# Kernel tuning notes

Hardware: AMD Instinct MI355X
Metric: run time of the kernel (lower is better)

Reference implementation:

```python
import jax, jax.numpy as jnp
import numpy as np

P, Q = 4, 16            # mlp_quad_last_shape
N, D_IN, H = 100000, 3, 256
N_QUAD = 128


def setup_inputs() -> dict:
    key = jax.random.key(0)
    ks = jax.random.split(key, 20)
    sc = lambda fan: 1.0 / np.sqrt(fan)
    inp = {}
    inp["input"] = jax.random.normal(ks[0], (N, D_IN), jnp.float32)
    inp["eq_param"] = jax.random.uniform(ks[1], (1,), jnp.float32)
    for i in range(5):
        inp[f"quad_x{i}"] = jax.random.uniform(ks[2 + i], (N_QUAD, 1), jnp.float32)
    # mlp_x params: Linear(3->256) -> tanh -> Linear(256->1024=P^5)
    inp["Wx1"] = jax.random.normal(ks[7], (D_IN, H), jnp.float32) * sc(D_IN)
    inp["bx1"] = jnp.zeros((H,), jnp.float32)
    inp["Wx2"] = jax.random.normal(ks[8], (H, P ** 5), jnp.float32) * sc(H)
    inp["bx2"] = jnp.zeros((P ** 5,), jnp.float32)
    # per-axis quad MLPs: Linear(1 -> P*Q)
    for i in range(5):
        inp[f"Wq{i}"] = jax.random.normal(ks[9 + i], (1, P * Q), jnp.float32) * sc(1)
        inp[f"bq{i}"] = jnp.zeros((P * Q,), jnp.float32)
    return inp


def reference(input, eq_param, quad_x0, quad_x1, quad_x2, quad_x3, quad_x4,
              Wx1, bx1, Wx2, bx2,
              Wq0, bq0, Wq1, bq1, Wq2, bq2, Wq3, bq3, Wq4, bq4):
    # lhs = mlp_x(input): [N, P^5]
    lhs = jnp.tanh(input @ Wx1 + bx1) @ Wx2 + bx2

    quads = (quad_x0, quad_x1, quad_x2, quad_x3, quad_x4)
    Ws = (Wq0, Wq1, Wq2, Wq3, Wq4)
    bs = (bq0, bq1, bq2, bq3, bq4)

    # Each factor: out_quad_i = y_i * (quad_x_i @ Wq_i + bq_i), reshape [n_i, P, Q].
    # The original einsum 'abx,cdx,efx,lmx,wvx->abcdeflmwv' followed by movedims,
    # reshape and sum over the merged n-axes is a multilinear map, so summing
    # each factor over its n_i axis FIRST gives the identical rhs tensor
    # (sum commutes with the outer product), avoiding the 10-D intermediate.
    ss = []
    for qx, W, b in zip(quads, Ws, bs):
        y = jnp.exp(-jnp.sum(qx * qx, axis=-1, keepdims=True) * eq_param[0])  # r_func weight [n_i,1]
        oq = (y * (qx @ W + b)).reshape(-1, P, Q)  # [n_i, P, Q]
        ss.append(jnp.sum(oq, axis=0))             # [P, Q]
    s0, s1, s2, s3, s4 = ss
    # rhs[b,d,f,m,v] = sum_x s0[b,x] s1[d,x] s2[f,x] s3[m,x] s4[v,x]  -> flatten to [P^5]
    rhs = jnp.einsum('bx,dx,fx,mx,vx->bdfmv', s0, s1, s2, s3, s4).reshape(-1)
    return lhs @ rhs  # [N]
```

## Files before the change

### kernel.cpp

```cpp
#include <hip/hip_runtime.h>

#define QQ 16
#define NQ 128
#define HH 256
#define P5 1024
#define LOG2E   1.44269504088896340f
#define K2LOG2E 2.88539008177792681f

__device__ __forceinline__ float block_sum256(float v, float* red, int t) {
#pragma unroll
  for (int o = 32; o > 0; o >>= 1) v += __shfl_down(v, o, 64);
  if ((t & 63) == 0) red[t >> 6] = v;
  __syncthreads();
  float r = red[0] + red[1] + red[2] + red[3];
  __syncthreads();
  return r;
}

__global__ __launch_bounds__(256) void prep_kernel(
    const float* __restrict__ eq,
    const float* __restrict__ q0, const float* __restrict__ q1,
    const float* __restrict__ q2, const float* __restrict__ q3,
    const float* __restrict__ q4,
    const float* __restrict__ Wx2, const float* __restrict__ bx2,
    const float* __restrict__ Wq0, const float* __restrict__ bq0,
    const float* __restrict__ Wq1, const float* __restrict__ bq1,
    const float* __restrict__ Wq2, const float* __restrict__ bq2,
    const float* __restrict__ Wq3, const float* __restrict__ bq3,
    const float* __restrict__ Wq4, const float* __restrict__ bq4,
    float* __restrict__ ws) {
  __shared__ float sS[5][64];
  __shared__ float sRhs[P5];
  __shared__ float sPart[4][10];
  __shared__ float sAB[10];
  __shared__ float red[4];

  const int t = threadIdx.x;
  const int hb = blockIdx.x;
  const float c = -eq[0] * LOG2E;

  const float* qs[5]  = {q0, q1, q2, q3, q4};
  const float* Wqs[5] = {Wq0, Wq1, Wq2, Wq3, Wq4};
  const float* bqs[5] = {bq0, bq1, bq2, bq3, bq4};

  float v[10];
#pragma unroll
  for (int i = 0; i < 5; ++i) {
    float a = 0.f, b = 0.f;
    if (t < NQ) {
      float x = qs[i][t];
      float y = exp2f(x * x * c);
      a = y * x;
      b = y;
    }
    v[2 * i] = a;
    v[2 * i + 1] = b;
  }
#pragma unroll
  for (int k = 0; k < 10; ++k) {
    float s = v[k];
#pragma unroll
    for (int o = 32; o > 0; o >>= 1) s += __shfl_down(s, o, 64);
    if ((t & 63) == 0) sPart[t >> 6][k] = s;
  }
  __syncthreads();
  if (t < 10) sAB[t] = sPart[0][t] + sPart[1][t] + sPart[2][t] + sPart[3][t];
  __syncthreads();

  for (int k = t; k < 5 * 64; k += 256) {
    int i = k >> 6, j = k & 63;
    sS[i][j] = Wqs[i][j] * sAB[2 * i] + bqs[i][j] * sAB[2 * i + 1];
  }
  __syncthreads();

  for (int idx = t; idx < P5; idx += 256) {
    int b = (idx >> 8) & 3, d = (idx >> 6) & 3, f = (idx >> 4) & 3,
        m = (idx >> 2) & 3, w = idx & 3;
    float s = 0.f;
#pragma unroll
    for (int x = 0; x < QQ; ++x)
      s += sS[0][b * QQ + x] * sS[1][d * QQ + x] * sS[2][f * QQ + x] *
           sS[3][m * QQ + x] * sS[4][w * QQ + x];
    sRhs[idx] = s;
  }
  __syncthreads();

  const float* wrow = Wx2 + hb * P5;
  float p = 0.f;
#pragma unroll
  for (int k = 0; k < 4; ++k)
    p = fmaf(wrow[t + 256 * k], sRhs[t + 256 * k], p);
  p = block_sum256(p, red, t);
  if (t == 0) ws[hb] = p;

  if (hb == 0) {
    float pb = 0.f;
    for (int j = t; j < P5; j += 256) pb = fmaf(bx2[j], sRhs[j], pb);
    pb = block_sum256(pb, red, t);
    if (t == 0) ws[HH] = pb;
  }
}

__global__ __launch_bounds__(256) void main_kernel(
    const float* __restrict__ input, const float* __restrict__ Wx1,
    const float* __restrict__ bx1, const float* __restrict__ wsv,
    float* __restrict__ out, int n) {
  __shared__ float4 qtab[HH];
  __shared__ float4 wtabv[HH / 4];
  __shared__ float red[4];

  const int t = threadIdx.x;

  float w2r = wsv[t];
  qtab[t] = make_float4(K2LOG2E * Wx1[t], K2LOG2E * Wx1[HH + t],
                        K2LOG2E * Wx1[2 * HH + t], K2LOG2E * bx1[t]);
  ((float*)wtabv)[t] = -2.0f * w2r;

  float s = w2r;
#pragma unroll
  for (int o = 32; o > 0; o >>= 1) s += __shfl_down(s, o, 64);
  if ((t & 63) == 0) red[t >> 6] = s;
  __syncthreads();
  const float CONST = red[0] + red[1] + red[2] + red[3] + wsv[HH];

  const int rA = blockIdx.x * 512 + t;
  const int rB = rA + 256;
  const bool vA = rA < n, vB = rB < n;
  float xa0 = 0.f, xa1 = 0.f, xa2 = 0.f;
  float xb0 = 0.f, xb1 = 0.f, xb2 = 0.f;
  if (vA) { xa0 = input[rA * 3]; xa1 = input[rA * 3 + 1]; xa2 = input[rA * 3 + 2]; }
  if (vB) { xb0 = input[rB * 3]; xb1 = input[rB * 3 + 1]; xb2 = input[rB * 3 + 2]; }

  float accA = 0.f, accB = 0.f;
#pragma unroll 4
  for (int h4 = 0; h4 < HH / 4; ++h4) {
    const float4 wq = wtabv[h4];
    const float wrv[4] = {wq.x, wq.y, wq.z, wq.w};
#pragma unroll
    for (int u = 0; u < 4; ++u) {
      const float4 q = qtab[h4 * 4 + u];
      float aA = fmaf(q.z, xa2, fmaf(q.y, xa1, fmaf(q.x, xa0, q.w)));
      float aB = fmaf(q.z, xb2, fmaf(q.y, xb1, fmaf(q.x, xb0, q.w)));
      float eA = exp2f(aA);
      float eB = exp2f(aB);
      float rA_ = __builtin_amdgcn_rcpf(eA + 1.0f);
      float rB_ = __builtin_amdgcn_rcpf(eB + 1.0f);
      accA = fmaf(wrv[u], rA_, accA);
      accB = fmaf(wrv[u], rB_, accB);
    }
  }

  if (vA) out[rA] = accA + CONST;
  if (vB) out[rB] = accB + CONST;
}

extern "C" void kernel_launch(void* const* d_in, const int* in_sizes, int n_in,
                              void* d_out, int out_size, void* d_ws,
                              size_t ws_size, hipStream_t stream) {
  const float* input = (const float*)d_in[0];
  const float* eq    = (const float*)d_in[1];
  const float* q0    = (const float*)d_in[2];
  const float* q1    = (const float*)d_in[3];
  const float* q2    = (const float*)d_in[4];
  const float* q3    = (const float*)d_in[5];
  const float* q4    = (const float*)d_in[6];
  const float* Wx1   = (const float*)d_in[7];
  const float* bx1   = (const float*)d_in[8];
  const float* Wx2   = (const float*)d_in[9];
  const float* bx2   = (const float*)d_in[10];
  const float* Wq0   = (const float*)d_in[11];
  const float* bq0   = (const float*)d_in[12];
  const float* Wq1   = (const float*)d_in[13];
  const float* bq1   = (const float*)d_in[14];
  const float* Wq2   = (const float*)d_in[15];
  const float* bq2   = (const float*)d_in[16];
  const float* Wq3   = (const float*)d_in[17];
  const float* bq3   = (const float*)d_in[18];
  const float* Wq4   = (const float*)d_in[19];
  const float* bq4   = (const float*)d_in[20];

  float* ws  = (float*)d_ws;
  float* out = (float*)d_out;
  const int n = in_sizes[0] / 3;

  hipLaunchKernelGGL(prep_kernel, dim3(HH), dim3(256), 0, stream,
                     eq, q0, q1, q2, q3, q4, Wx2, bx2,
                     Wq0, bq0, Wq1, bq1, Wq2, bq2, Wq3, bq3, Wq4, bq4, ws);

  const int blocks = (n + 511) / 512;
  hipLaunchKernelGGL(main_kernel, dim3(blocks), dim3(256), 0, stream,
                     input, Wx1, bx1, ws, out, n);
}
```

Baseline: 119.6 us.

## Split hidden dimension across waves and precompute scaled weight tables in prep

```diff
diff --git a/kernel.cpp b/kernel.cpp
--- a/kernel.cpp
+++ b/kernel.cpp
@@ -22,6 +22,7 @@
     const float* __restrict__ q0, const float* __restrict__ q1,
     const float* __restrict__ q2, const float* __restrict__ q3,
     const float* __restrict__ q4,
+    const float* __restrict__ Wx1, const float* __restrict__ bx1,
     const float* __restrict__ Wx2, const float* __restrict__ bx2,
     const float* __restrict__ Wq0, const float* __restrict__ bq0,
     const float* __restrict__ Wq1, const float* __restrict__ bq1,
@@ -91,67 +92,92 @@
   for (int k = 0; k < 4; ++k)
     p = fmaf(wrow[t + 256 * k], sRhs[t + 256 * k], p);
   p = block_sum256(p, red, t);
-  if (t == 0) ws[hb] = p;
+
+  if (t == 0) {
+    ws[hb]          = K2LOG2E * Wx1[hb];
+    ws[HH + hb]     = K2LOG2E * Wx1[HH + hb];
+    ws[2 * HH + hb] = K2LOG2E * Wx1[2 * HH + hb];
+    ws[3 * HH + hb] = K2LOG2E * bx1[hb];
+    ws[4 * HH + hb] = -2.0f * p;
+  }
 
   if (hb == 0) {
     float pb = 0.f;
     for (int j = t; j < P5; j += 256) pb = fmaf(bx2[j], sRhs[j], pb);
     pb = block_sum256(pb, red, t);
-    if (t == 0) ws[HH] = pb;
+    if (t == 0) ws[5 * HH] = pb;
   }
 }
 
 __global__ __launch_bounds__(256) void main_kernel(
-    const float* __restrict__ input, const float* __restrict__ Wx1,
-    const float* __restrict__ bx1, const float* __restrict__ wsv,
+    const float* __restrict__ input, const float* __restrict__ ws,
     float* __restrict__ out, int n) {
   __shared__ float4 qtab[HH];
-  __shared__ float4 wtabv[HH / 4];
+  __shared__ float4 wtab4[HH / 4];
   __shared__ float red[4];
+  __shared__ float sred[4][4][64];
 
   const int t = threadIdx.x;
-
-  float w2r = wsv[t];
-  qtab[t] = make_float4(K2LOG2E * Wx1[t], K2LOG2E * Wx1[HH + t],
-                        K2LOG2E * Wx1[2 * HH + t], K2LOG2E * bx1[t]);
-  ((float*)wtabv)[t] = -2.0f * w2r;
-
-  float s = w2r;
-#pragma unroll
-  for (int o = 32; o > 0; o >>= 1) s += __shfl_down(s, o, 64);
-  if ((t & 63) == 0) red[t >> 6] = s;
-  __syncthreads();
-  const float CONST = red[0] + red[1] + red[2] + red[3] + wsv[HH];
-
-  const int rA = blockIdx.x * 512 + t;
-  const int rB = rA + 256;
-  const bool vA = rA < n, vB = rB < n;
-  float xa0 = 0.f, xa1 = 0.f, xa2 = 0.f;
-  float xb0 = 0.f, xb1 = 0.f, xb2 = 0.f;
-  if (vA) { xa0 = input[rA * 3]; xa1 = input[rA * 3 + 1]; xa2 = input[rA * 3 + 2]; }
-  if (vB) { xb0 = input[rB * 3]; xb1 = input[rB * 3 + 1]; xb2 = input[rB * 3 + 2]; }
-
-  float accA = 0.f, accB = 0.f;
+  const int lane = t & 63;
+  const int wv = t >> 6;
+
+  const float w0 = ws[t], w1 = ws[HH + t], w2 = ws[2 * HH + t];
+  const float bb = ws[3 * HH + t], wr = ws[4 * HH + t];
+  qtab[t] = make_float4(w0, w1, w2, bb);
+  ((float*)wtab4)[t] = wr;
+
+  float s = wr;
+#pragma unroll
+  for (int o = 32; o > 0; o >>= 1) s += __shfl_xor(s, o, 64);
+  if (lane == 0) red[wv] = s;
+  __syncthreads();
+  const float CONST = fmaf(-0.5f, (red[0] + red[1]) + (red[2] + red[3]),
+                           ws[5 * HH]);
+
+  const int row0 = blockIdx.x * 256;
+  float x0[4], x1[4], x2[4], acc[4];
+#pragma unroll
+  for (int r = 0; r < 4; ++r) {
+    const int row = row0 + r * 64 + lane;
+    x0[r] = x1[r] = x2[r] = 0.f;
+    if (row < n) {
+      x0[r] = input[row * 3 + 0];
+      x1[r] = input[row * 3 + 1];
+      x2[r] = input[row * 3 + 2];
+    }
+    acc[r] = 0.f;
+  }
+
+  const int hbase = wv * 64;
 #pragma unroll 4
-  for (int h4 = 0; h4 < HH / 4; ++h4) {
-    const float4 wq = wtabv[h4];
+  for (int j = 0; j < 16; ++j) {
+    const float4 wq = wtab4[wv * 16 + j];
     const float wrv[4] = {wq.x, wq.y, wq.z, wq.w};
 #pragma unroll
     for (int u = 0; u < 4; ++u) {
-      const float4 q = qtab[h4 * 4 + u];
-      float aA = fmaf(q.z, xa2, fmaf(q.y, xa1, fmaf(q.x, xa0, q.w)));
-      float aB = fmaf(q.z, xb2, fmaf(q.y, xb1, fmaf(q.x, xb0, q.w)));
-      float eA = exp2f(aA);
-      float eB = exp2f(aB);
-      float rA_ = __builtin_amdgcn_rcpf(eA + 1.0f);
-      float rB_ = __builtin_amdgcn_rcpf(eB + 1.0f);
-      accA = fmaf(wrv[u], rA_, accA);
-      accB = fmaf(wrv[u], rB_, accB);
-    }
-  }
-
-  if (vA) out[rA] = accA + CONST;
-  if (vB) out[rB] = accB + CONST;
+      const float4 q = qtab[hbase + j * 4 + u];
+#pragma unroll
+      for (int r = 0; r < 4; ++r) {
+        float a = fmaf(q.z, x2[r], fmaf(q.y, x1[r], fmaf(q.x, x0[r], q.w)));
+        float rc = __builtin_amdgcn_rcpf(exp2f(a) + 1.0f);
+        acc[r] = fmaf(wrv[u], rc, acc[r]);
+      }
+    }
+  }
+
+#pragma unroll
+  for (int r = 0; r < 4; ++r) sred[wv][r][lane] = acc[r];
+  __syncthreads();
+
+  {
+    const int rr = wv;
+    const int row = row0 + rr * 64 + lane;
+    if (row < n) {
+      float sum = (sred[0][rr][lane] + sred[1][rr][lane]) +
+                  (sred[2][rr][lane] + sred[3][rr][lane]);
+      out[row] = sum + CONST;
+    }
+  }
 }
 
 extern "C" void kernel_launch(void* const* d_in, const int* in_sizes, int n_in,
@@ -184,10 +210,10 @@
   const int n = in_sizes[0] / 3;
 
   hipLaunchKernelGGL(prep_kernel, dim3(HH), dim3(256), 0, stream,
-                     eq, q0, q1, q2, q3, q4, Wx2, bx2,
+                     eq, q0, q1, q2, q3, q4, Wx1, bx1, Wx2, bx2,
                      Wq0, bq0, Wq1, bq1, Wq2, bq2, Wq3, bq3, Wq4, bq4, ws);
 
-  const int blocks = (n + 511) / 512;
+  const int blocks = (n + 255) / 256;
   hipLaunchKernelGGL(main_kernel, dim3(blocks), dim3(256), 0, stream,
-                     input, Wx1, bx1, ws, out, n);
-}
+                     input, ws, out, n);
+}
```

Measured after the change: 115.8 us. -3.2%, faster.
